# Optimization experiments

Hardware: AMD Instinct MI355X
Metric: run time of the kernel (lower is better)

The kernel has to match this reference:

```python
import jax, jax.numpy as jnp
import numpy as np

ANG = 7
N = ANG * ANG          # 49 views
CENTER = N // 2        # index 24 = central view
EDGE_C = 150.0
ALPHA = 0.1
CROP = 8
GAUSS = jnp.array([[0.0751, 0.1238, 0.0751],
                   [0.1238, 0.2042, 0.1238],
                   [0.0751, 0.1238, 0.0751]], dtype=jnp.float32)


def _edge_aware_smoothness(D, I):
    # D: [b,h,w] disparity; I: [b,3,h,w] center view
    gx = I[:, :, :, 1:] - I[:, :, :, :-1]
    gy = I[:, :, 1:, :] - I[:, :, :-1, :]
    wx = jnp.exp(-EDGE_C * jnp.mean(jnp.abs(gx), axis=1, keepdims=True))
    wy = jnp.exp(-EDGE_C * jnp.mean(jnp.abs(gy), axis=1, keepdims=True))
    Du = D[:, None]
    dgx = Du[:, :, :, 1:] - Du[:, :, :, :-1]
    dgy = Du[:, :, 1:, :] - Du[:, :, :-1, :]
    lx = jnp.mean((wx * jnp.abs(dgx))[:, :, CROP:-CROP, CROP:-CROP])
    ly = jnp.mean((wy * jnp.abs(dgy))[:, :, CROP:-CROP, CROP:-CROP])
    return (lx + ly) / 2.0


def _warp_all(pred, x):
    # Backward-warp each of the 49 views toward the center view using the
    # per-pixel disparity scaled by the view's angular offset (bilinear,
    # border-clamped) -- standard light-field warping (warp_all in the repo).
    # pred: [b,h,w]; x: [b,3,N,h,w] -> warped [b,3,N,h,w]
    b, c, n, h, w = x.shape
    off = jnp.arange(ANG, dtype=pred.dtype) - (ANG // 2)
    du = jnp.repeat(off, ANG)   # row (u) offset per view, [N]
    dv = jnp.tile(off, ANG)     # col (v) offset per view, [N]
    gy = jnp.arange(h, dtype=pred.dtype)[:, None]
    gx = jnp.arange(w, dtype=pred.dtype)[None, :]
    p = pred[:, None, :, :]                                # [b,1,h,w]
    cy = jnp.clip(gy[None, None] + p * du[None, :, None, None], 0.0, h - 1)
    cx = jnp.clip(gx[None, None] + p * dv[None, :, None, None], 0.0, w - 1)
    y0f = jnp.floor(cy); x0f = jnp.floor(cx)
    ty = (cy - y0f)[..., None]; tx = (cx - x0f)[..., None]
    y0 = y0f.astype(jnp.int32); x0 = x0f.astype(jnp.int32)
    y1 = jnp.minimum(y0 + 1, h - 1); x1 = jnp.minimum(x0 + 1, w - 1)
    img = jnp.transpose(x, (0, 2, 3, 4, 1)).reshape(b, n, h * w, c)

    def gather(yi, xi):
        idx = (yi * w + xi).reshape(b, n, h * w, 1)
        return jnp.take_along_axis(img, idx, axis=2).reshape(b, n, h, w, c)

    out = (gather(y0, x0) * (1 - ty) * (1 - tx)
           + gather(y0, x1) * (1 - ty) * tx
           + gather(y1, x0) * ty * (1 - tx)
           + gather(y1, x1) * ty * tx)
    return jnp.transpose(out, (0, 4, 1, 2, 3))


def _gauss_smooth_angular(cl):
    # cl [b,1,N,h,w]: 3x3 gaussian conv over the 7x7 angular grid, replicate pad
    b, _, _, h, w = cl.shape
    g = cl.reshape(b, 1, ANG, ANG, h, w)
    g = jnp.pad(g, ((0, 0), (0, 0), (1, 1), (1, 1), (0, 0), (0, 0)), mode='edge')
    out = sum(GAUSS[i, j] * g[:, :, i:i + ANG, j:j + ANG]
              for i in range(3) for j in range(3))
    return out.reshape(b, 1, N, h, w)


def _forward(pred, x, y, epoch):
    b, u, v, h, w, c = x.shape
    # 'b u v h w c -> b c (u v) h w'
    xr = jnp.transpose(x, (0, 5, 1, 2, 3, 4)).reshape(b, c, N, h, w)
    center = xr[:, :, CENTER]                               # [b,3,h,w]
    grad_loss = _edge_aware_smoothness(pred, center)
    warped = _warp_all(pred, xr)                            # [b,3,N,h,w]
    color_loss = jnp.mean(jnp.abs(warped - warped[:, :, CENTER:CENTER + 1]),
                          axis=1, keepdims=True)            # [b,1,N,h,w]
    if epoch > 0:
        gauss = jax.lax.stop_gradient(_gauss_smooth_angular(color_loss))
        idx = jnp.argsort(-gauss, axis=2)                   # descending
        sorted_cl = jnp.take_along_axis(color_loss, idx, axis=2)
    else:
        sorted_cl = -jnp.sort(-color_loss, axis=2)
    yb = y[:, None, None, :, :]
    ar = jnp.arange(N, dtype=y.dtype)[None, None, :, None, None]
    mask = (ar > yb).astype(color_loss.dtype) / (N - yb) * N
    if epoch > 0:
        mask = jax.lax.stop_gradient(mask)                  # torch no_grad branch
    cl = jnp.mean((sorted_cl * mask)[..., CROP:-CROP, CROP:-CROP])
    return cl + grad_loss * ALPHA


def setup_inputs():
    key = jax.random.key(0)
    k1, k2, k3 = jax.random.split(key, 3)
    b, h, w = 4, 256, 256
    pred = jax.random.normal(k1, (b, h, w), dtype=jnp.float32)
    x = jax.random.uniform(k2, (b, ANG, ANG, h, w, 3), dtype=jnp.float32)
    y = jax.random.uniform(k3, (b, h, w), dtype=jnp.float32) * 24.0  # keep ~half views
    return {"pred": pred, "x": x, "y": y, "epoch": 5}


def reference(pred, x, y, epoch):
    return _forward(pred, x, y, epoch)
```

## Files before the change

### kernel.cpp

```cpp
#include <hip/hip_runtime.h>
#include <math.h>

#define NV    49
#define Himg  256
#define Wimg  256
#define RW    240
#define RWH   (RW*RW)
#define NPIX  (4*RWH)
#define ROWF  (Wimg*3)
#define IMGF  (Himg*Wimg*3)
#define NBLK  (NPIX/64)


#define CL7(a) ((a)<0?0:((a)>6?6:(a)))

#define DO_VIEW(UC, VC) { \
    const float* s0p = xv + ((UC)*7 + (VC)) * IMGF + ro0 + co[VC]; \
    const float* s1p = xv + ((UC)*7 + (VC)) * IMGF + ro1 + co[VC]; \
    float s0[6], s1[6]; \
    __builtin_memcpy(s0, s0p, 24); \
    __builtin_memcpy(s1, s1p, 24); \
    float tx = txv[VC]; \
    float h0 = s0[0] + tx*(s0[3]-s0[0]); \
    float h1 = s0[1] + tx*(s0[4]-s0[1]); \
    float h2 = s0[2] + tx*(s0[5]-s0[2]); \
    float k0 = s1[0] + tx*(s1[3]-s1[0]); \
    float k1 = s1[1] + tx*(s1[4]-s1[1]); \
    float k2 = s1[2] + tx*(s1[5]-s1[2]); \
    float o0 = h0 + ty*(k0-h0); \
    float o1 = h1 + ty*(k1-h1); \
    float o2 = h2 + ty*(k2-h2); \
    mycl[(UC)*7+(VC)] = (fabsf(o0-c0)+fabsf(o1-c1)+fabsf(o2-c2)) * (1.0f/3.0f); \
}

#define DO_U(UC) { \
    float cy = fminf(fmaxf((float)yy + p * (float)((UC)-3), 0.0f), 255.0f); \
    float y0f = floorf(cy); \
    float ty = cy - y0f; \
    int iy0 = (int)y0f; \
    int iy1 = min(iy0+1, 255); \
    int ro0 = iy0*ROWF, ro1 = iy1*ROWF; \
    DO_VIEW(UC,0) DO_VIEW(UC,1) DO_VIEW(UC,2) DO_VIEW(UC,3) \
    DO_VIEW(UC,4) DO_VIEW(UC,5) DO_VIEW(UC,6) \
}

#define GV(UC,VC) myg[(UC)*7+(VC)] = \
    0.0751f*mycl[CL7((UC)-1)*7+CL7((VC)-1)] + 0.1238f*mycl[CL7((UC)-1)*7+(VC)] + 0.0751f*mycl[CL7((UC)-1)*7+CL7((VC)+1)] + \
    0.1238f*mycl[(UC)*7+CL7((VC)-1)]        + 0.2042f*mycl[(UC)*7+(VC)]        + 0.1238f*mycl[(UC)*7+CL7((VC)+1)] + \
    0.0751f*mycl[CL7((UC)+1)*7+CL7((VC)-1)] + 0.1238f*mycl[CL7((UC)+1)*7+(VC)] + 0.0751f*mycl[CL7((UC)+1)*7+CL7((VC)+1)];

#define GU(UC) GV(UC,0) GV(UC,1) GV(UC,2) GV(UC,3) GV(UC,4) GV(UC,5) GV(UC,6)

__global__ __launch_bounds__(256) void color_kernel(
    const float* __restrict__ pred, const float* __restrict__ x,
    const float* __restrict__ y, const int* __restrict__ epoch_p,
    double* __restrict__ acc)
{
    __shared__ float s_cl[64 * NV];
    __shared__ float s_g [64 * NV];
    __shared__ float sred[4];

    const int tid = threadIdx.x;
    const int pix = tid & 63;
    const int sub = tid >> 6;

    int lb  = (blockIdx.x & 7) * (NBLK/8) + (blockIdx.x >> 3);
    int pid = lb * 64 + pix;
    int b   = pid / RWH;
    int rem = pid - b * RWH;
    int ry  = rem / RW;
    int yy  = 8 + ry;
    int xx  = 8 + (rem - ry * RW);

    int pidx = (b * Himg + yy) * Wimg + xx;
    float p = pred[pidx];

    const float* xv    = x + (size_t)b * (49 * IMGF);
    const float* cbase = xv + (24 * IMGF) + (yy * Wimg + xx) * 3;
    float c0 = cbase[0], c1 = cbase[1], c2 = cbase[2];

    float* mycl = s_cl + pix * NV;
    float* myg  = s_g  + pix * NV;

    int co[7]; float txv[7];
    #pragma unroll
    for (int vv = 0; vv < 7; vv++) {
        float cx = fminf(fmaxf((float)xx + p * (float)(vv-3), 0.0f), 255.0f);
        float x0f = floorf(cx);
        float tx = cx - x0f;
        int ix0 = (int)x0f;
        if (ix0 >= 255) { ix0 = 254; tx = 1.0f; }
        co[vv] = ix0 * 3; txv[vv] = tx;
    }

    if (sub == 0)      { DO_U(0) DO_U(4) }
    else if (sub == 1) { DO_U(1) DO_U(5) }
    else if (sub == 2) { DO_U(2) DO_U(6) }
    else {
        DO_U(3)
        float lx = 0.0f, ly = 0.0f;
        if (xx <= 246) {
            float q6[6]; __builtin_memcpy(q6, cbase, 24);
            float wx = __expf(-50.0f * (fabsf(q6[3]-c0) + fabsf(q6[4]-c1) + fabsf(q6[5]-c2)));
            lx = wx * fabsf(pred[pidx + 1] - p);
        }
        if (yy <= 246) {
            float r0 = cbase[ROWF], r1 = cbase[ROWF+1], r2 = cbase[ROWF+2];
            float wy = __expf(-50.0f * (fabsf(r0-c0) + fabsf(r1-c1) + fabsf(r2-c2)));
            ly = wy * fabsf(pred[pidx + Wimg] - p);
        }
        #pragma unroll
        for (int off = 32; off > 0; off >>= 1) {
            lx += __shfl_down(lx, off);
            ly += __shfl_down(ly, off);
        }
        if ((tid & 63) == 0) {
            atomicAdd(acc + 1, (double)lx);
            atomicAdd(acc + 2, (double)ly);
        }
    }
    __syncthreads();

    const int epoch = *epoch_p;

    if (epoch > 0) {
        if (sub == 0)      { GU(0) GU(4) }
        else if (sub == 1) { GU(1) GU(5) }
        else if (sub == 2) { GU(2) GU(6) }
        else               { GU(3) }
    }
    __syncthreads();

    const float* key = (epoch > 0) ? myg : mycl;
    float yval = y[pidx];

    unsigned long long kn[13];
    int cnt[13];
    #pragma unroll
    for (int i = 0; i < 13; i++) {
        int n = sub + 4*i;
        if (n < NV) {
            unsigned int bb = __float_as_uint(key[n]);
            kn[i] = (((unsigned long long)bb) << 8) | (unsigned long long)(255 - n);
        } else kn[i] = ~0ULL;
        cnt[i] = 0;
    }
    for (int m = 0; m < NV; m++) {
        unsigned int bm = __float_as_uint(key[m]);
        unsigned long long km = (((unsigned long long)bm) << 8) | (unsigned long long)(255 - m);
        #pragma unroll
        for (int i = 0; i < 13; i++)
            cnt[i] += (km > kn[i]) ? 1 : 0;
    }
    float tail = 0.0f;
    #pragma unroll
    for (int i = 0; i < 13; i++) {
        int n = sub + 4*i;
        if (n < NV)
            tail += ((float)cnt[i] > yval) ? mycl[n] : 0.0f;
    }
    float contrib = tail * (49.0f / (49.0f - yval));

    #pragma unroll
    for (int off = 32; off > 0; off >>= 1)
        contrib += __shfl_down(contrib, off);
    if ((tid & 63) == 0) sred[sub] = contrib;
    __syncthreads();
    if (tid == 0)
        atomicAdd(acc + 0, (double)(sred[0] + sred[1] + sred[2] + sred[3]));
}

__global__ void finalize_kernel(const double* __restrict__ acc,
                                float* __restrict__ out)
{
    double cl = acc[0] / 11289600.0;
    double gl = (acc[1] + acc[2]) / (2.0 * 229440.0);
    out[0] = (float)(cl + 0.1 * gl);
}

extern "C" void kernel_launch(void* const* d_in, const int* in_sizes, int n_in,
                              void* d_out, int out_size, void* d_ws, size_t ws_size,
                              hipStream_t stream)
{
    const float* pred  = (const float*)d_in[0];
    const float* x     = (const float*)d_in[1];
    const float* y     = (const float*)d_in[2];
    const int*   epoch = (const int*)d_in[3];
    double* acc = (double*)d_ws;

    hipMemsetAsync(acc, 0, 3 * sizeof(double), stream);
    color_kernel<<<NBLK, 256, 0, stream>>>(pred, x, y, epoch, acc);
    finalize_kernel<<<1, 1, 0, stream>>>(acc, (float*)d_out);
}
```

Baseline: 325.5 us.

## Compute all 49 views per thread in registers, dropping shared-memory staging

Instead of four threads per pixel that split the views and exchange per-view losses through shared memory, each thread now handles one pixel completely. All 49 color losses, the angular Gaussian and the rank counting live in registers, and the 64-bit packed-key comparison becomes float compares with index tie-breaking. This removes shared memory traffic and intra-block syncs and cuts the number of atomics per pixel, but it greatly raises register pressure (two 49-float arrays plus a fully unrolled 49x49 compare) and gives four times fewer threads to hide the gather latency.

Measured after the change: 455.8 us. 1.4x slower.

```diff
diff --git a/kernel.cpp b/kernel.cpp
--- a/kernel.cpp
+++ b/kernel.cpp
@@ -9,165 +9,139 @@
 #define NPIX  (4*RWH)
 #define ROWF  (Wimg*3)
 #define IMGF  (Himg*Wimg*3)
-#define NBLK  (NPIX/64)
-
+#define BLK   128
+#define NBLK  (NPIX/BLK)
 
 #define CL7(a) ((a)<0?0:((a)>6?6:(a)))
 
-#define DO_VIEW(UC, VC) { \
-    const float* s0p = xv + ((UC)*7 + (VC)) * IMGF + ro0 + co[VC]; \
-    const float* s1p = xv + ((UC)*7 + (VC)) * IMGF + ro1 + co[VC]; \
-    float s0[6], s1[6]; \
-    __builtin_memcpy(s0, s0p, 24); \
-    __builtin_memcpy(s1, s1p, 24); \
-    float tx = txv[VC]; \
-    float h0 = s0[0] + tx*(s0[3]-s0[0]); \
-    float h1 = s0[1] + tx*(s0[4]-s0[1]); \
-    float h2 = s0[2] + tx*(s0[5]-s0[2]); \
-    float k0 = s1[0] + tx*(s1[3]-s1[0]); \
-    float k1 = s1[1] + tx*(s1[4]-s1[1]); \
-    float k2 = s1[2] + tx*(s1[5]-s1[2]); \
-    float o0 = h0 + ty*(k0-h0); \
-    float o1 = h1 + ty*(k1-h1); \
-    float o2 = h2 + ty*(k2-h2); \
-    mycl[(UC)*7+(VC)] = (fabsf(o0-c0)+fabsf(o1-c1)+fabsf(o2-c2)) * (1.0f/3.0f); \
-}
-
-#define DO_U(UC) { \
-    float cy = fminf(fmaxf((float)yy + p * (float)((UC)-3), 0.0f), 255.0f); \
-    float y0f = floorf(cy); \
-    float ty = cy - y0f; \
-    int iy0 = (int)y0f; \
-    int iy1 = min(iy0+1, 255); \
-    int ro0 = iy0*ROWF, ro1 = iy1*ROWF; \
-    DO_VIEW(UC,0) DO_VIEW(UC,1) DO_VIEW(UC,2) DO_VIEW(UC,3) \
-    DO_VIEW(UC,4) DO_VIEW(UC,5) DO_VIEW(UC,6) \
-}
-
-#define GV(UC,VC) myg[(UC)*7+(VC)] = \
-    0.0751f*mycl[CL7((UC)-1)*7+CL7((VC)-1)] + 0.1238f*mycl[CL7((UC)-1)*7+(VC)] + 0.0751f*mycl[CL7((UC)-1)*7+CL7((VC)+1)] + \
-    0.1238f*mycl[(UC)*7+CL7((VC)-1)]        + 0.2042f*mycl[(UC)*7+(VC)]        + 0.1238f*mycl[(UC)*7+CL7((VC)+1)] + \
-    0.0751f*mycl[CL7((UC)+1)*7+CL7((VC)-1)] + 0.1238f*mycl[CL7((UC)+1)*7+(VC)] + 0.0751f*mycl[CL7((UC)+1)*7+CL7((VC)+1)];
-
-#define GU(UC) GV(UC,0) GV(UC,1) GV(UC,2) GV(UC,3) GV(UC,4) GV(UC,5) GV(UC,6)
-
-__global__ __launch_bounds__(256) void color_kernel(
+__global__ __launch_bounds__(BLK) void loss_kernel(
     const float* __restrict__ pred, const float* __restrict__ x,
     const float* __restrict__ y, const int* __restrict__ epoch_p,
     double* __restrict__ acc)
 {
-    __shared__ float s_cl[64 * NV];
-    __shared__ float s_g [64 * NV];
-    __shared__ float sred[4];
+    __shared__ float sred[2][3];
+    const int tid = threadIdx.x;
 
-    const int tid = threadIdx.x;
-    const int pix = tid & 63;
-    const int sub = tid >> 6;
-
-    int lb  = (blockIdx.x & 7) * (NBLK/8) + (blockIdx.x >> 3);
-    int pid = lb * 64 + pix;
+    int lb  = (blockIdx.x & 7) * (NBLK / 8) + (blockIdx.x >> 3);
+    int pid = lb * BLK + tid;
     int b   = pid / RWH;
     int rem = pid - b * RWH;
     int ry  = rem / RW;
     int yy  = 8 + ry;
     int xx  = 8 + (rem - ry * RW);
 
-    int pidx = (b * Himg + yy) * Wimg + xx;
-    float p = pred[pidx];
+    int   pidx = (b * Himg + yy) * Wimg + xx;
+    float p    = pred[pidx];
 
     const float* xv    = x + (size_t)b * (49 * IMGF);
-    const float* cbase = xv + (24 * IMGF) + (yy * Wimg + xx) * 3;
+    const float* cbase = xv + 24 * IMGF + (yy * Wimg + xx) * 3;
     float c0 = cbase[0], c1 = cbase[1], c2 = cbase[2];
 
-    float* mycl = s_cl + pix * NV;
-    float* myg  = s_g  + pix * NV;
-
-    int co[7]; float txv[7];
+    int ro0[7], ro1[7]; float tyv[7];
+    int co[7];          float txv[7];
     #pragma unroll
-    for (int vv = 0; vv < 7; vv++) {
-        float cx = fminf(fmaxf((float)xx + p * (float)(vv-3), 0.0f), 255.0f);
+    for (int u = 0; u < 7; u++) {
+        float cy  = fminf(fmaxf((float)yy + p * (float)(u - 3), 0.0f), 255.0f);
+        float y0f = floorf(cy);
+        tyv[u] = cy - y0f;
+        int iy0 = (int)y0f;
+        ro0[u] = iy0 * ROWF;
+        ro1[u] = min(iy0 + 1, 255) * ROWF;
+    }
+    #pragma unroll
+    for (int v = 0; v < 7; v++) {
+        float cx  = fminf(fmaxf((float)xx + p * (float)(v - 3), 0.0f), 255.0f);
         float x0f = floorf(cx);
-        float tx = cx - x0f;
-        int ix0 = (int)x0f;
+        float tx  = cx - x0f;
+        int   ix0 = (int)x0f;
         if (ix0 >= 255) { ix0 = 254; tx = 1.0f; }
-        co[vv] = ix0 * 3; txv[vv] = tx;
+        co[v] = ix0 * 3; txv[v] = tx;
     }
 
-    if (sub == 0)      { DO_U(0) DO_U(4) }
-    else if (sub == 1) { DO_U(1) DO_U(5) }
-    else if (sub == 2) { DO_U(2) DO_U(6) }
-    else {
-        DO_U(3)
-        float lx = 0.0f, ly = 0.0f;
-        if (xx <= 246) {
-            float q6[6]; __builtin_memcpy(q6, cbase, 24);
-            float wx = __expf(-50.0f * (fabsf(q6[3]-c0) + fabsf(q6[4]-c1) + fabsf(q6[5]-c2)));
-            lx = wx * fabsf(pred[pidx + 1] - p);
-        }
-        if (yy <= 246) {
-            float r0 = cbase[ROWF], r1 = cbase[ROWF+1], r2 = cbase[ROWF+2];
-            float wy = __expf(-50.0f * (fabsf(r0-c0) + fabsf(r1-c1) + fabsf(r2-c2)));
-            ly = wy * fabsf(pred[pidx + Wimg] - p);
-        }
+    float cl[NV];
+    #pragma unroll
+    for (int u = 0; u < 7; u++) {
         #pragma unroll
-        for (int off = 32; off > 0; off >>= 1) {
-            lx += __shfl_down(lx, off);
-            ly += __shfl_down(ly, off);
-        }
-        if ((tid & 63) == 0) {
-            atomicAdd(acc + 1, (double)lx);
-            atomicAdd(acc + 2, (double)ly);
+        for (int v = 0; v < 7; v++) {
+            const float* base = xv + (u * 7 + v) * IMGF;
+            float s0[6], s1[6];
+            __builtin_memcpy(s0, base + ro0[u] + co[v], 24);
+            __builtin_memcpy(s1, base + ro1[u] + co[v], 24);
+            float tx = txv[v], ty = tyv[u];
+            float h0 = s0[0] + tx * (s0[3] - s0[0]);
+            float h1 = s0[1] + tx * (s0[4] - s0[1]);
+            float h2 = s0[2] + tx * (s0[5] - s0[2]);
+            float k0 = s1[0] + tx * (s1[3] - s1[0]);
+            float k1 = s1[1] + tx * (s1[4] - s1[1]);
+            float k2 = s1[2] + tx * (s1[5] - s1[2]);
+            float o0 = h0 + ty * (k0 - h0);
+            float o1 = h1 + ty * (k1 - h1);
+            float o2 = h2 + ty * (k2 - h2);
+            cl[u * 7 + v] = (fabsf(o0 - c0) + fabsf(o1 - c1) + fabsf(o2 - c2))
+                            * (1.0f / 3.0f);
         }
     }
-    __syncthreads();
+
+    float lx = 0.0f, ly = 0.0f;
+    if (xx <= 246) {
+        float q3 = cbase[3], q4 = cbase[4], q5 = cbase[5];
+        float wx = __expf(-50.0f * (fabsf(q3 - c0) + fabsf(q4 - c1) + fabsf(q5 - c2)));
+        lx = wx * fabsf(pred[pidx + 1] - p);
+    }
+    if (yy <= 246) {
+        float r0 = cbase[ROWF], r1 = cbase[ROWF + 1], r2 = cbase[ROWF + 2];
+        float wy = __expf(-50.0f * (fabsf(r0 - c0) + fabsf(r1 - c1) + fabsf(r2 - c2)));
+        ly = wy * fabsf(pred[pidx + Wimg] - p);
+    }
 
     const int epoch = *epoch_p;
+    float g[NV];
+    if (epoch > 0) {
+        #pragma unroll
+        for (int u = 0; u < 7; u++) {
+            #pragma unroll
+            for (int v = 0; v < 7; v++) {
+                g[u * 7 + v] =
+                    0.0751f * cl[CL7(u-1)*7 + CL7(v-1)] + 0.1238f * cl[CL7(u-1)*7 + v] + 0.0751f * cl[CL7(u-1)*7 + CL7(v+1)] +
+                    0.1238f * cl[u*7 + CL7(v-1)]        + 0.2042f * cl[u*7 + v]        + 0.1238f * cl[u*7 + CL7(v+1)] +
+                    0.0751f * cl[CL7(u+1)*7 + CL7(v-1)] + 0.1238f * cl[CL7(u+1)*7 + v] + 0.0751f * cl[CL7(u+1)*7 + CL7(v+1)];
+            }
+        }
+    } else {
+        #pragma unroll
+        for (int n = 0; n < NV; n++) g[n] = cl[n];
+    }
 
-    if (epoch > 0) {
-        if (sub == 0)      { GU(0) GU(4) }
-        else if (sub == 1) { GU(1) GU(5) }
-        else if (sub == 2) { GU(2) GU(6) }
-        else               { GU(3) }
-    }
-    __syncthreads();
-
-    const float* key = (epoch > 0) ? myg : mycl;
     float yval = y[pidx];
-
-    unsigned long long kn[13];
-    int cnt[13];
-    #pragma unroll
-    for (int i = 0; i < 13; i++) {
-        int n = sub + 4*i;
-        if (n < NV) {
-            unsigned int bb = __float_as_uint(key[n]);
-            kn[i] = (((unsigned long long)bb) << 8) | (unsigned long long)(255 - n);
-        } else kn[i] = ~0ULL;
-        cnt[i] = 0;
-    }
-    for (int m = 0; m < NV; m++) {
-        unsigned int bm = __float_as_uint(key[m]);
-        unsigned long long km = (((unsigned long long)bm) << 8) | (unsigned long long)(255 - m);
-        #pragma unroll
-        for (int i = 0; i < 13; i++)
-            cnt[i] += (km > kn[i]) ? 1 : 0;
-    }
     float tail = 0.0f;
     #pragma unroll
-    for (int i = 0; i < 13; i++) {
-        int n = sub + 4*i;
-        if (n < NV)
-            tail += ((float)cnt[i] > yval) ? mycl[n] : 0.0f;
+    for (int n = 0; n < NV; n++) {
+        int cnt = 0;
+        #pragma unroll
+        for (int m = 0; m < NV; m++) {
+            if (m < n)      cnt += (g[m] >= g[n]) ? 1 : 0;
+            else if (m > n) cnt += (g[m] >  g[n]) ? 1 : 0;
+        }
+        tail += ((float)cnt > yval) ? cl[n] : 0.0f;
     }
     float contrib = tail * (49.0f / (49.0f - yval));
 
     #pragma unroll
-    for (int off = 32; off > 0; off >>= 1)
+    for (int off = 32; off > 0; off >>= 1) {
         contrib += __shfl_down(contrib, off);
-    if ((tid & 63) == 0) sred[sub] = contrib;
+        lx      += __shfl_down(lx, off);
+        ly      += __shfl_down(ly, off);
+    }
+    int wid = tid >> 6;
+    if ((tid & 63) == 0) {
+        sred[wid][0] = contrib; sred[wid][1] = lx; sred[wid][2] = ly;
+    }
     __syncthreads();
-    if (tid == 0)
-        atomicAdd(acc + 0, (double)(sred[0] + sred[1] + sred[2] + sred[3]));
+    if (tid == 0) {
+        atomicAdd(acc + 0, (double)(sred[0][0] + sred[1][0]));
+        atomicAdd(acc + 1, (double)(sred[0][1] + sred[1][1]));
+        atomicAdd(acc + 2, (double)(sred[0][2] + sred[1][2]));
+    }
 }
 
 __global__ void finalize_kernel(const double* __restrict__ acc,
@@ -189,6 +163,6 @@
     double* acc = (double*)d_ws;
 
     hipMemsetAsync(acc, 0, 3 * sizeof(double), stream);
-    color_kernel<<<NBLK, 256, 0, stream>>>(pred, x, y, epoch, acc);
+    loss_kernel<<<NBLK, BLK, 0, stream>>>(pred, x, y, epoch, acc);
     finalize_kernel<<<1, 1, 0, stream>>>(acc, (float*)d_out);
 }
```
